# Kernel tuning notes

Hardware: AMD Instinct MI355X
Metric: run time of the kernel (lower is better)

Reference implementation:

```python
import jax, jax.numpy as jnp
import numpy as np

B, S, D, K = 2, 4096, 512, 32
EPS = 1e-8


def _cantor_measure(n, levels=24):
    """Devil's staircase (Cantor function) evaluated at i/(n-1)."""
    t = np.arange(n, dtype=np.float64) / max(n - 1, 1)
    c = np.zeros(n)
    r = t.copy()
    done = np.zeros(n, dtype=bool)
    scale = 0.5
    for _ in range(levels):
        r = r * 3.0
        d = np.clip(np.floor(r).astype(np.int64), 0, 2)
        r = r - d
        add = np.where(d == 2, scale, 0.0) + np.where(d == 1, scale, 0.0)
        c = np.where(done, c, c + add)
        done = done | (d == 1)
        scale *= 0.5
    return c


def _build_routes_and_weights(n, k):
    """Cantor-distance k-nearest routing (seq_len, k) and normalized fusion weights."""
    c = _cantor_measure(n)
    dist = np.abs(c[:, None] - c[None, :])  # (S, S), built once on host
    idx = np.argsort(dist, axis=1, kind='stable')[:, :k].astype(np.int32)
    d = np.take_along_axis(dist, idx, axis=1)
    w = np.exp(-d)  # geometric 'weighted' fusion mode
    w = w / (w.sum(axis=1, keepdims=True) + EPS)
    return idx, w.astype(np.float32)


def setup_inputs() -> dict:
    key = jax.random.key(0)
    k1, k2, k3, k4 = jax.random.split(key, 4)
    routes_np, weights_np = _build_routes_and_weights(S, K)
    return {
        'x': jax.random.normal(k1, (B, S, D), dtype=jnp.float32),
        'W_in': jax.random.normal(k2, (D, D), dtype=jnp.float32) * (1.0 / np.sqrt(D)),
        'W_out': jax.random.normal(k3, (D, D), dtype=jnp.float32) * (1.0 / np.sqrt(D)),
        'b_out': jax.random.normal(k4, (D,), dtype=jnp.float32) * 0.02,
        'fusion_weights': jnp.asarray(weights_np),
        'routes': jnp.asarray(routes_np),
    }


def reference(x, W_in, W_out, b_out, fusion_weights, routes):
    # 1. input projection (bias-free), heads are a contiguous split of D so
    #    the shared per-position weights make the per-head fuse equal to a flat fuse
    h = x @ W_in                                  # (B, S, D)
    # 2. gather fusion window per position (irregular Cantor routing)
    g = jnp.take(h, routes, axis=1)               # (B, S, K, D)
    # 3. weighted fusion with normalized staircase-distance weights
    fused = jnp.einsum('bskd,sk->bsd', g, fusion_weights)
    # 4. output projection + residual
    out = fused @ W_out + b_out
    return x + out
```

## Files before the change

### kernel.cpp

```cpp
#include <hip/hip_runtime.h>
#include <hip/hip_bf16.h>
#include <stdint.h>

#define S_LEN  4096
#define D_DIM  512
#define K_R    32
#define M_ROWS 8192

typedef __attribute__((ext_vector_type(8))) short bf16x8;
typedef __attribute__((ext_vector_type(4))) float f32x4;

__device__ __forceinline__ float bf2f(short u) {
  union { unsigned int i; float f; } c;
  c.i = ((unsigned int)(unsigned short)u) << 16;
  return c.f;
}

__device__ __forceinline__ void gload_lds16(const void* g, void* lds) {
  __builtin_amdgcn_global_load_lds(
      (__attribute__((address_space(1))) void*)g,
      (__attribute__((address_space(3))) void*)lds, 16, 0, 0);
}

__device__ __forceinline__ int4 pack8(float4 v0, float4 v1) {
  union { __hip_bfloat16 h[8]; int4 v; } u;
  u.h[0] = __float2bfloat16(v0.x); u.h[1] = __float2bfloat16(v0.y);
  u.h[2] = __float2bfloat16(v0.z); u.h[3] = __float2bfloat16(v0.w);
  u.h[4] = __float2bfloat16(v1.x); u.h[5] = __float2bfloat16(v1.y);
  u.h[6] = __float2bfloat16(v1.z); u.h[7] = __float2bfloat16(v1.w);
  return u.v;
}

__global__ void __launch_bounds__(256) prep_kernel(
    const float* __restrict__ x, __hip_bfloat16* __restrict__ xb,
    const float* __restrict__ Win, __hip_bfloat16* __restrict__ Winb,
    const float* __restrict__ Wout, __hip_bfloat16* __restrict__ WoutTb) {
  __shared__ __hip_bfloat16 Lds[64][66];
  const int tid = threadIdx.x;
  if (blockIdx.x < 2048) {
    const int lin = blockIdx.x;
    const int chunk = (lin & 7) * 256 + (lin >> 3);
    const int i = chunk * 256 + tid;
    const float4* xp = (const float4*)x;
    ((int4*)xb)[i] = pack8(xp[2 * i], xp[2 * i + 1]);
    return;
  }
  if (blockIdx.x < 2112) {
    const int e4 = ((blockIdx.x - 2048) * 256 + tid) * 4;
    const float4* wp = (const float4*)Win;
    int4* op = (int4*)Winb;
#pragma unroll
    for (int h = 0; h < 2; ++h)
      op[e4 / 2 + h] = pack8(wp[e4 + 2 * h], wp[e4 + 2 * h + 1]);
    return;
  }
  const int bx = blockIdx.x - 2112;
  const int tr = (bx >> 3) * 64;
  const int tc = (bx & 7) * 64;
#pragma unroll
  for (int it = 0; it < 4; ++it) {
    const int id = it * 256 + tid;
    const int r = id >> 4, c4 = (id & 15) * 4;
    const float4 v = *(const float4*)&Wout[(size_t)(tr + r) * 512 + tc + c4];
    Lds[r][c4]     = __float2bfloat16(v.x);
    Lds[r][c4 + 1] = __float2bfloat16(v.y);
    Lds[r][c4 + 2] = __float2bfloat16(v.z);
    Lds[r][c4 + 3] = __float2bfloat16(v.w);
  }
  __syncthreads();
#pragma unroll
  for (int it = 0; it < 2; ++it) {
    const int id = it * 256 + tid;
    const int j = id >> 3, i0 = (id & 7) * 8;
    union { __hip_bfloat16 h[8]; int4 v; } u;
#pragma unroll
    for (int r = 0; r < 8; ++r) u.h[r] = Lds[i0 + r][j];
    *(int4*)&WoutTb[(size_t)(tc + j) * 512 + tr + i0] = u.v;
  }
}

#define BM 128
#define BN 64
#define BK 64

__global__ void __launch_bounds__(256) mid_kernel(
    const __hip_bfloat16* __restrict__ xb,
    const float* __restrict__ fw,
    const int* __restrict__ routes,
    __hip_bfloat16* __restrict__ g,
    const __hip_bfloat16* __restrict__ WoutTb,
    const __hip_bfloat16* __restrict__ Winb,
    __hip_bfloat16* __restrict__ WcT) {
  __shared__ __hip_bfloat16 As[BM][BK];
  __shared__ __hip_bfloat16 Bs[BN][BK];
  __shared__ float w_s[4][K_R];
  __shared__ int   r_s[4][K_R];
  const int tid = threadIdx.x;
  const int w = tid >> 6, l = tid & 63;

  if (blockIdx.x >= 32) {
    const int lin = blockIdx.x - 32;
    const int bchunk = (lin & 7) * 256 + (lin >> 3);
    const int row = bchunk * 4 + w;
    const int s = row & (S_LEN - 1);
    const int b = row >> 12;
    if (l < K_R) {
      r_s[w][l] = routes[s * K_R + l];
      w_s[w][l] = fw[s * K_R + l];
    }
    __syncthreads();
    const __hip_bfloat16* xbb = xb + (size_t)b * S_LEN * D_DIM + l * 8;
    float acc[8] = {};
#pragma unroll 8
    for (int k = 0; k < K_R; ++k) {
      const float wk = w_s[w][k];
      const bf16x8 v = *(const bf16x8*)(xbb + (size_t)r_s[w][k] * D_DIM);
#pragma unroll
      for (int j = 0; j < 8; ++j) acc[j] = fmaf(wk, bf2f(v[j]), acc[j]);
    }
    union { __hip_bfloat16 h[8]; int4 v; } u;
#pragma unroll
    for (int j = 0; j < 8; ++j) u.h[j] = __float2bfloat16(acc[j]);
    *(int4*)(g + (size_t)row * D_DIM + l * 8) = u.v;
    return;
  }

  const int id2 = blockIdx.x;
  const int bm0 = (id2 >> 3) * BM;
  const int bn0 = (id2 & 7) * BN;
  const int wr  = (w >> 1) * 64;
  const int wcn = (w & 1) * 32;

  const int rin = l >> 3;
  const int usw = (l & 7) ^ rin;
  const __hip_bfloat16* gA = WoutTb + (size_t)(bm0 + w * 8 + rin) * D_DIM + usw * 8;
  const __hip_bfloat16* gB = Winb   + (size_t)(bn0 + w * 8 + rin) * D_DIM + usw * 8;
  __hip_bfloat16* ldsA = &As[w * 8][0];
  __hip_bfloat16* ldsB = &Bs[w * 8][0];
  const int fr = l & 15, fq = l >> 4;

  f32x4 acc[4][2] = {};
  for (int k0 = 0; k0 < D_DIM; k0 += BK) {
#pragma unroll
    for (int i = 0; i < 4; ++i)
      gload_lds16(gA + (size_t)(i * 32) * D_DIM + k0, ldsA + i * 32 * BK);
#pragma unroll
    for (int j = 0; j < 2; ++j)
      gload_lds16(gB + (size_t)(j * 32) * D_DIM + k0, ldsB + j * 32 * BK);
    __syncthreads();
#pragma unroll
    for (int kk = 0; kk < 2; ++kk) {
      const int u = (kk * 4 + fq) ^ (fr & 7);
      bf16x8 af[4], bfv[2];
#pragma unroll
      for (int m = 0; m < 4; ++m)
        af[m] = *(const bf16x8*)&As[wr + m * 16 + fr][u * 8];
#pragma unroll
      for (int n = 0; n < 2; ++n)
        bfv[n] = *(const bf16x8*)&Bs[wcn + n * 16 + fr][u * 8];
#pragma unroll
      for (int m = 0; m < 4; ++m)
#pragma unroll
        for (int n = 0; n < 2; ++n)
          acc[m][n] = __builtin_amdgcn_mfma_f32_16x16x32_bf16(af[m], bfv[n], acc[m][n], 0, 0, 0);
    }
    __syncthreads();
  }
#pragma unroll
  for (int m = 0; m < 4; ++m)
#pragma unroll
    for (int n = 0; n < 2; ++n)
#pragma unroll
      for (int r = 0; r < 4; ++r) {
        const int grow = bm0 + wr + m * 16 + fq * 4 + r;
        const int gcol = bn0 + wcn + n * 16 + fr;
        WcT[(size_t)grow * D_DIM + gcol] = __float2bfloat16(acc[m][n][r]);
      }
}

#define GBN 128

__global__ void __launch_bounds__(512, 4) gemm_out_kernel(
    const __hip_bfloat16* __restrict__ A,
    const __hip_bfloat16* __restrict__ BT,
    const float* __restrict__ x,
    const float* __restrict__ b_out,
    float* __restrict__ out) {
  __shared__ __hip_bfloat16 As[2][BM][BK];
  __shared__ __hip_bfloat16 Bs[2][GBN][BK];
  const int tid = threadIdx.x;
  const int w = tid >> 6, l = tid & 63;

  const int bid = blockIdx.x;
  const int id2 = (bid & 7) * 32 + (bid >> 3);
  const int bm0 = (id2 >> 2) * BM;
  const int bn0 = (id2 & 3) * GBN;

  const int wr  = (w >> 2) * 64;
  const int wcn = (w & 3) * 32;

  const int rin = l >> 3;
  const int usw = (l & 7) ^ rin;
  const __hip_bfloat16* gA = A + (size_t)(bm0 + w * 16 + rin) * D_DIM + usw * 8;
  const __hip_bfloat16* gB = BT + (size_t)(bn0 + w * 16 + rin) * D_DIM + usw * 8;

  const int fr = l & 15, fq = l >> 4;
  f32x4 acc[4][2] = {};

#define STAGE(buf, k0)                                                          \
  {                                                                             \
    _Pragma("unroll")                                                           \
    for (int i = 0; i < 2; ++i)                                                 \
      gload_lds16(gA + (size_t)(i * 8) * D_DIM + (k0),                          \
                  &As[buf][w * 16 + i * 8][0]);                                 \
    _Pragma("unroll")                                                           \
    for (int j = 0; j < 2; ++j)                                                 \
      gload_lds16(gB + (size_t)(j * 8) * D_DIM + (k0),                          \
                  &Bs[buf][w * 16 + j * 8][0]);                                 \
  }

#define COMPUTE(buf)                                                            \
  {                                                                             \
    _Pragma("unroll")                                                           \
    for (int kk = 0; kk < 2; ++kk) {                                            \
      const int u = (kk * 4 + fq) ^ (fr & 7);                                   \
      bf16x8 af[4], bfv[2];                                                     \
      _Pragma("unroll")                                                         \
      for (int m = 0; m < 4; ++m)                                               \
        af[m] = *(const bf16x8*)&As[buf][wr + m * 16 + fr][u * 8];              \
      _Pragma("unroll")                                                         \
      for (int n = 0; n < 2; ++n)                                               \
        bfv[n] = *(const bf16x8*)&Bs[buf][wcn + n * 16 + fr][u * 8];            \
      _Pragma("unroll")                                                         \
      for (int m = 0; m < 4; ++m)                                               \
        _Pragma("unroll")                                                       \
        for (int n = 0; n < 2; ++n)                                             \
          acc[m][n] = __builtin_amdgcn_mfma_f32_16x16x32_bf16(                  \
              af[m], bfv[n], acc[m][n], 0, 0, 0);                               \
    }                                                                           \
  }

  STAGE(0, 0);
#pragma unroll
  for (int t = 0; t < 7; ++t) {
    STAGE((t + 1) & 1, (t + 1) * BK);
    asm volatile("s_waitcnt vmcnt(4)" ::: "memory");
    __builtin_amdgcn_s_barrier();
    __builtin_amdgcn_sched_barrier(0);
    COMPUTE(t & 1);
    __builtin_amdgcn_s_barrier();
  }
  asm volatile("s_waitcnt vmcnt(0)" ::: "memory");
  __builtin_amdgcn_s_barrier();
  __builtin_amdgcn_sched_barrier(0);
  COMPUTE(1);
#undef STAGE
#undef COMPUTE

  const float bb0 = b_out[bn0 + wcn + fr];
  const float bb1 = b_out[bn0 + wcn + 16 + fr];
#pragma unroll
  for (int m = 0; m < 4; ++m)
#pragma unroll
    for (int r = 0; r < 4; ++r) {
      const int grow = bm0 + wr + m * 16 + fq * 4 + r;
      const size_t base = (size_t)grow * D_DIM + bn0 + wcn + fr;
      out[base]      = acc[m][0][r] + x[base]      + bb0;
      out[base + 16] = acc[m][1][r] + x[base + 16] + bb1;
    }
}

extern "C" void kernel_launch(void* const* d_in, const int* in_sizes, int n_in,
                              void* d_out, int out_size, void* d_ws, size_t ws_size,
                              hipStream_t stream) {
  const float* x      = (const float*)d_in[0];
  const float* W_in   = (const float*)d_in[1];
  const float* W_out  = (const float*)d_in[2];
  const float* b_out  = (const float*)d_in[3];
  const float* fw     = (const float*)d_in[4];
  const int*   routes = (const int*)d_in[5];
  float* out = (float*)d_out;

  char* ws = (char*)d_ws;
  __hip_bfloat16* Xb     = (__hip_bfloat16*)ws;
  __hip_bfloat16* WcT    = (__hip_bfloat16*)(ws + 8388608);
  __hip_bfloat16* g      = (__hip_bfloat16*)(ws + 8912896);
  __hip_bfloat16* Winb   = (__hip_bfloat16*)(ws + 17301504);
  __hip_bfloat16* WoutTb = (__hip_bfloat16*)(ws + 17825792);

  prep_kernel<<<2176, 256, 0, stream>>>(x, Xb, W_in, Winb, W_out, WoutTb);
  mid_kernel<<<2080, 256, 0, stream>>>(Xb, fw, routes, g, WoutTb, Winb, WcT);
  gemm_out_kernel<<<256, 512, 0, stream>>>(g, WcT, x, b_out, out);
}
```

Baseline: 35.15 us.

## Share gathered rows across eight positions via a dense weight table

New measurement: 46.33 us. +31.8%, slower.

```diff
diff --git a/kernel.cpp b/kernel.cpp
--- a/kernel.cpp
+++ b/kernel.cpp
@@ -93,35 +93,80 @@
     __hip_bfloat16* __restrict__ WcT) {
   __shared__ __hip_bfloat16 As[BM][BK];
   __shared__ __hip_bfloat16 Bs[BN][BK];
-  __shared__ float w_s[4][K_R];
-  __shared__ int   r_s[4][K_R];
+  __shared__ int   r_s[8][32];
+  __shared__ float w_s[8][32];
+  __shared__ float w_tab[64][8];
+  __shared__ int lo_s, hi_s;
   const int tid = threadIdx.x;
   const int w = tid >> 6, l = tid & 63;
 
   if (blockIdx.x >= 32) {
     const int lin = blockIdx.x - 32;
-    const int bchunk = (lin & 7) * 256 + (lin >> 3);
-    const int row = bchunk * 4 + w;
-    const int s = row & (S_LEN - 1);
-    const int b = row >> 12;
-    if (l < K_R) {
-      r_s[w][l] = routes[s * K_R + l];
-      w_s[w][l] = fw[s * K_R + l];
-    }
-    __syncthreads();
-    const __hip_bfloat16* xbb = xb + (size_t)b * S_LEN * D_DIM + l * 8;
-    float acc[8] = {};
-#pragma unroll 8
-    for (int k = 0; k < K_R; ++k) {
-      const float wk = w_s[w][k];
-      const bf16x8 v = *(const bf16x8*)(xbb + (size_t)r_s[w][k] * D_DIM);
-#pragma unroll
-      for (int j = 0; j < 8; ++j) acc[j] = fmaf(wk, bf2f(v[j]), acc[j]);
-    }
-    union { __hip_bfloat16 h[8]; int4 v; } u;
-#pragma unroll
-    for (int j = 0; j < 8; ++j) u.h[j] = __float2bfloat16(acc[j]);
-    *(int4*)(g + (size_t)row * D_DIM + l * 8) = u.v;
+    const int bchunk = (lin & 7) * 128 + (lin >> 3);
+    const int r0 = bchunk * 8;
+    const int s0 = r0 & (S_LEN - 1);
+    const int b = r0 >> 12;
+    if (tid == 0) { lo_s = 0x7fffffff; hi_s = -1; }
+    __syncthreads();
+    {
+      const int rl = tid >> 5, k = tid & 31;
+      const int rt = routes[(s0 + rl) * K_R + k];
+      const float wk = fw[(s0 + rl) * K_R + k];
+      r_s[rl][k] = rt;
+      w_s[rl][k] = wk;
+      atomicMin(&lo_s, rt);
+      atomicMax(&hi_s, rt);
+      ((float2*)w_tab)[tid] = make_float2(0.f, 0.f);
+    }
+    __syncthreads();
+    const int lo = lo_s;
+    const int span = hi_s - lo + 1;
+    const bool tabbed = (span <= 64);
+    if (tabbed) {
+      const int rl = tid >> 5, k = tid & 31;
+      w_tab[r_s[rl][k] - lo][rl] = w_s[rl][k];
+    }
+    __syncthreads();
+
+    const __hip_bfloat16* xbat = xb + (size_t)b * S_LEN * D_DIM;
+    const int w2 = w * 2;
+    float acc0[8] = {}, acc1[8] = {};
+    if (tabbed) {
+      for (int r = 0; r < span; ++r) {
+        const float wk0 = w_tab[r][w2];
+        const float wk1 = w_tab[r][w2 + 1];
+        if (wk0 == 0.f && wk1 == 0.f) continue;
+        const bf16x8 v = *(const bf16x8*)(xbat + (size_t)(lo + r) * D_DIM + l * 8);
+        float f[8];
+#pragma unroll
+        for (int j = 0; j < 8; ++j) f[j] = bf2f(v[j]);
+#pragma unroll
+        for (int j = 0; j < 8; ++j) {
+          acc0[j] = fmaf(wk0, f[j], acc0[j]);
+          acc1[j] = fmaf(wk1, f[j], acc1[j]);
+        }
+      }
+    } else {
+#pragma unroll 4
+      for (int k = 0; k < K_R; ++k) {
+        const float wk0 = w_s[w2][k];
+        const bf16x8 v0 = *(const bf16x8*)(xbat + (size_t)r_s[w2][k] * D_DIM + l * 8);
+#pragma unroll
+        for (int j = 0; j < 8; ++j) acc0[j] = fmaf(wk0, bf2f(v0[j]), acc0[j]);
+        const float wk1 = w_s[w2 + 1][k];
+        const bf16x8 v1 = *(const bf16x8*)(xbat + (size_t)r_s[w2 + 1][k] * D_DIM + l * 8);
+#pragma unroll
+        for (int j = 0; j < 8; ++j) acc1[j] = fmaf(wk1, bf2f(v1[j]), acc1[j]);
+      }
+    }
+    union { __hip_bfloat16 h[8]; int4 v; } u0, u1;
+#pragma unroll
+    for (int j = 0; j < 8; ++j) {
+      u0.h[j] = __float2bfloat16(acc0[j]);
+      u1.h[j] = __float2bfloat16(acc1[j]);
+    }
+    *(int4*)(g + (size_t)(r0 + w2) * D_DIM + l * 8)     = u0.v;
+    *(int4*)(g + (size_t)(r0 + w2 + 1) * D_DIM + l * 8) = u1.v;
     return;
   }
 
@@ -289,6 +334,6 @@
   __hip_bfloat16* WoutTb = (__hip_bfloat16*)(ws + 17825792);
 
   prep_kernel<<<2176, 256, 0, stream>>>(x, Xb, W_in, Winb, W_out, WoutTb);
-  mid_kernel<<<2080, 256, 0, stream>>>(Xb, fw, routes, g, WoutTb, Winb, WcT);
+  mid_kernel<<<1056, 256, 0, stream>>>(Xb, fw, routes, g, WoutTb, Winb, WcT);
   gemm_out_kernel<<<256, 512, 0, stream>>>(g, WcT, x, b_out, out);
 }
```
